# Kernel optimization log

Measured on AMD Instinct MI355X. Metric: run time of the kernel, lower is better.

Reference implementation:

```python
import jax, jax.numpy as jnp
import numpy as np
from jax import lax

D_MODEL = 1024
D_STATE = 128
D_CONV = 4
EXPAND = 2
N_HEADS = 32
CHUNK = 64
D_INNER = EXPAND * D_MODEL                 # 2048
CONV_DIM = D_INNER + 2 * D_STATE           # 2304
D_IN_PROJ = 2 * D_INNER + 2 * D_STATE + N_HEADS  # 4384
HEAD_DIM = D_INNER // N_HEADS              # 64
EPS = 1e-5


def setup_inputs() -> dict:
    key = jax.random.key(0)
    ks = jax.random.split(key, 10)
    u = jax.random.normal(ks[0], (4, 4096, D_MODEL), dtype=jnp.float32)
    in_proj_w = jax.random.normal(ks[1], (D_IN_PROJ, D_MODEL), dtype=jnp.float32) * 0.02
    conv_w = jax.random.normal(ks[2], (CONV_DIM, 1, D_CONV), dtype=jnp.float32) * 0.3
    conv_b = jnp.zeros((CONV_DIM,), dtype=jnp.float32)
    dt_bias = jax.random.uniform(ks[3], (N_HEADS,), minval=-0.5, maxval=0.5, dtype=jnp.float32)
    A_log = jax.random.uniform(ks[4], (N_HEADS,), minval=-0.1, maxval=-0.01, dtype=jnp.float32)
    D = jax.random.uniform(ks[5], (N_HEADS,), minval=0.9, maxval=1.1, dtype=jnp.float32)
    norm_w = jnp.ones((D_INNER,), dtype=jnp.float32)
    out_proj_w = jax.random.normal(ks[6], (D_MODEL, D_INNER), dtype=jnp.float32) * 0.02
    return {"u": u, "in_proj_w": in_proj_w, "conv_w": conv_w, "conv_b": conv_b,
            "dt_bias": dt_bias, "A_log": A_log, "D": D, "norm_w": norm_w,
            "out_proj_w": out_proj_w}


def segsum(x):
    """Stable segment sum. x: (..., T) -> (..., T, T); exp of it is 1-semiseparable."""
    T = x.shape[-1]
    xe = jnp.broadcast_to(x[..., :, None], x.shape + (T,))  # '... d -> ... d e'
    mask_strict = jnp.tril(jnp.ones((T, T), dtype=bool), k=-1)
    xe = jnp.where(mask_strict, xe, 0.0)
    seg = jnp.cumsum(xe, axis=-2)
    mask_incl = jnp.tril(jnp.ones((T, T), dtype=bool), k=0)
    return jnp.where(mask_incl, seg, -jnp.inf)


def ssd(x, A, B, C):
    """x:(b,L,h,p)  A:(b,L,h)  B,C:(b,L,h,n). L multiple of CHUNK."""
    b, Lp, h, p = x.shape
    n = B.shape[-1]
    c = Lp // CHUNK
    x = x.reshape(b, c, CHUNK, h, p)
    A = A.reshape(b, c, CHUNK, h).transpose(0, 3, 1, 2)       # (b,h,c,l)
    B = B.reshape(b, c, CHUNK, h, n)
    C = C.reshape(b, c, CHUNK, h, n)
    A_cumsum = jnp.cumsum(A, axis=-1)                          # (b,h,c,l)
    L = jnp.exp(segsum(A))                                     # (b,h,c,l,l)
    # intra-chunk (diagonal blocks)
    Y_diag = jnp.einsum('bclhn,bcshn,bhcls,bcshp->bclhp', C, B, L, x)
    # chunk-final states
    decay_states = jnp.exp(A_cumsum[:, :, :, -1:] - A_cumsum)  # (b,h,c,l)
    states = jnp.einsum('bclhn,bhcl,bclhp->bchpn', B, decay_states, x)
    init = jnp.zeros_like(states[:, :1])
    states = jnp.concatenate([init, states], axis=1)           # (b,c+1,h,p,n)
    decay_chunk = jnp.exp(segsum(jnp.pad(A_cumsum[:, :, :, -1], ((0, 0), (0, 0), (1, 0)))))
    new_states = jnp.einsum('bhzc,bchpn->bzhpn', decay_chunk, states)
    states, final_state = new_states[:, :-1], new_states[:, -1]
    # inter-chunk (off-diagonal) contribution
    state_decay_out = jnp.exp(A_cumsum)
    Y_off = jnp.einsum('bclhn,bchpn,bhcl->bclhp', C, states, state_decay_out)
    Y = (Y_diag + Y_off).reshape(b, Lp, h, p)
    return Y, final_state


def _forward(u, in_proj_w, conv_w, conv_b, dt_bias, A_log, D, norm_w, out_proj_w):
    b, seq_len, _ = u.shape
    pad = CHUNK - seq_len % CHUNK  # note: full extra chunk when seq_len % CHUNK == 0 (faithful)
    u = jnp.pad(u, ((0, 0), (0, pad), (0, 0)))
    Lp = u.shape[1]
    A = -jnp.exp(A_log)                                        # (h,)
    zxbcdt = jnp.einsum('bld,ed->ble', u, in_proj_w)           # (b,Lp,D_IN_PROJ)
    z = zxbcdt[..., :D_INNER]
    xBC = zxbcdt[..., D_INNER:D_INNER + CONV_DIM]
    dt = zxbcdt[..., -N_HEADS:]
    # causal depthwise conv1d + silu
    xc = xBC.transpose(0, 2, 1)                                # (b,conv_dim,Lp)
    xc = lax.conv_general_dilated(xc, conv_w, window_strides=(1,),
                                  padding=[(D_CONV - 1, 0)],
                                  feature_group_count=CONV_DIM,
                                  dimension_numbers=('NCH', 'OIH', 'NCH'))
    xBC = jax.nn.silu((xc + conv_b[None, :, None]).transpose(0, 2, 1))
    x = xBC[..., :D_INNER].reshape(b, Lp, N_HEADS, HEAD_DIM)
    Bm = xBC[..., D_INNER:D_INNER + D_STATE]
    Cm = xBC[..., D_INNER + D_STATE:]
    Bm = jnp.broadcast_to(Bm[:, :, None, :], (b, Lp, N_HEADS, D_STATE))
    Cm = jnp.broadcast_to(Cm[:, :, None, :], (b, Lp, N_HEADS, D_STATE))
    dt = jax.nn.softplus(dt + dt_bias)                         # (b,Lp,h)
    y, _ = ssd(x * dt[..., None], A * dt, Bm, Cm)
    y = y + x * D[None, None, :, None]
    y = y.reshape(b, Lp, D_INNER)
    # gated RMSNorm
    t = y * jax.nn.silu(z)
    t = t * jax.lax.rsqrt(jnp.mean(t * t, axis=-1, keepdims=True) + EPS) * norm_w
    out = jnp.einsum('bld,ed->ble', t, out_proj_w)
    return out[:, :seq_len]


def reference(u, in_proj_w, conv_w, conv_b, dt_bias, A_log, D, norm_w, out_proj_w):
    return _forward(u, in_proj_w, conv_w, conv_b, dt_bias, A_log, D, norm_w, out_proj_w)
```

## Files before the change

kernel.cpp:

```cpp
#include <hip/hip_runtime.h>
#include <hip/hip_bf16.h>
#include <math.h>


#define BL    16384
#define NCONV 2304
#define LDXP  2336

typedef __hip_bfloat16 bf16;
typedef __attribute__((ext_vector_type(8))) short bf16x8_i;
typedef __attribute__((ext_vector_type(4))) float f32x4;

union BF8 { uint4 u; bf16 h[8]; };
union BF2 { uint u; bf16 h[2]; };

__device__ __forceinline__ void gload_lds16(const void* g, void* l) {
  __builtin_amdgcn_global_load_lds(
      (__attribute__((address_space(1))) void*)(uintptr_t)g,
      (__attribute__((address_space(3))) void*)(uint32_t)(uintptr_t)l,
      16, 0, 0);
}

template<typename TC, bool CLAMPB>
__global__ __launch_bounds__(256) void gemm_bt_mfma(
    const bf16* __restrict__ A, int lda,
    const bf16* __restrict__ B, int ldb,
    TC* __restrict__ C, int ldc, int N, int K)
{
  __shared__ __align__(16) bf16 As2[2][128 * 64];
  __shared__ __align__(16) bf16 Bs2[2][128 * 64];
  const int tid  = threadIdx.x;
  const int lane = tid & 63;
  const int wid  = tid >> 6;

  const int gx  = gridDim.x;
  const int nwg = gx * gridDim.y;
  const int q   = nwg >> 3;
  int id = blockIdx.y * gx + blockIdx.x;
  id = (id & 7) * q + (id >> 3);
  const int bm = (id / gx) * 128;
  const int bn = (id % gx) * 128;

  const int wr = (wid >> 1) * 64;
  const int wc = (wid & 1) * 64;

  f32x4 acc[4][4] = {};

  int aoff[4][2], boff[4][2];
  #pragma unroll
  for (int i = 0; i < 4; ++i) {
    const int ar = wr + i * 16 + (lane & 15);
    const int br = wc + i * 16 + (lane & 15);
    const int asw = ((ar >> 1) & 7) << 3;
    const int bsw = ((br >> 1) & 7) << 3;
    #pragma unroll
    for (int ks = 0; ks < 2; ++ks) {
      const int c0 = ks * 32 + (lane >> 4) * 8;
      aoff[i][ks] = ar * 64 + (c0 ^ asw);
      boff[i][ks] = br * 64 + (c0 ^ bsw);
    }
  }

  const int srow = tid >> 3;
  const int sj   = tid & 7;
  const bf16* pA[4];
  const bf16* pB[4];
  #pragma unroll
  for (int i = 0; i < 4; ++i) {
    const int r  = i * 32 + srow;
    const int js = sj ^ ((r >> 1) & 7);
    int brow = bn + r;
    if (CLAMPB) brow = min(brow, N - 1);
    pA[i] = A + (size_t)(bm + r) * lda + js * 8;
    pB[i] = B + (size_t)brow * ldb + js * 8;
  }

  const int NT = K >> 6;
  #pragma unroll
  for (int i = 0; i < 4; ++i) {
    gload_lds16(pA[i], &As2[0][0] + i * 2048 + wid * 512);
    gload_lds16(pB[i], &Bs2[0][0] + i * 2048 + wid * 512);
    pA[i] += 64; pB[i] += 64;
  }

  for (int t = 0; t < NT; ++t) {
    const int cur = t & 1;
    if (t + 1 < NT) {
      bf16* dA = &As2[cur ^ 1][0];
      bf16* dB = &Bs2[cur ^ 1][0];
      #pragma unroll
      for (int i = 0; i < 4; ++i) {
        gload_lds16(pA[i], dA + i * 2048 + wid * 512);
        gload_lds16(pB[i], dB + i * 2048 + wid * 512);
        pA[i] += 64; pB[i] += 64;
      }
      asm volatile("s_waitcnt vmcnt(8)" ::: "memory");
    } else {
      asm volatile("s_waitcnt vmcnt(0)" ::: "memory");
    }
    __builtin_amdgcn_sched_barrier(0);
    __builtin_amdgcn_s_barrier();
    const bf16* Ab = &As2[cur][0];
    const bf16* Bb = &Bs2[cur][0];
    __builtin_amdgcn_s_setprio(1);
    #pragma unroll
    for (int ks = 0; ks < 2; ++ks) {
      bf16x8_i af[4], bfr[4];
      #pragma unroll
      for (int i = 0; i < 4; ++i) {
        af[i]  = *(const bf16x8_i*)(Ab + aoff[i][ks]);
        bfr[i] = *(const bf16x8_i*)(Bb + boff[i][ks]);
      }
      #pragma unroll
      for (int i = 0; i < 4; ++i)
        #pragma unroll
        for (int j = 0; j < 4; ++j)
          acc[i][j] = __builtin_amdgcn_mfma_f32_16x16x32_bf16(
              af[i], bfr[j], acc[i][j], 0, 0, 0);
    }
    __builtin_amdgcn_s_setprio(0);
    __builtin_amdgcn_s_barrier();
  }

  const int cr = (lane >> 4) * 4;
  const int cc = lane & 15;
  #pragma unroll
  for (int i = 0; i < 4; ++i) {
    #pragma unroll
    for (int j = 0; j < 4; ++j) {
      const int n = bn + wc + j * 16 + cc;
      if (n < N) {
        #pragma unroll
        for (int r = 0; r < 4; ++r) {
          const int m = bm + wr + i * 16 + cr + r;
          if constexpr (sizeof(TC) == 2)
            ((bf16*)C)[(size_t)m * ldc + n] = __float2bfloat16(acc[i][j][r]);
          else
            ((float*)C)[(size_t)m * ldc + n] = acc[i][j][r];
        }
      }
    }
  }
}

__global__ __launch_bounds__(256) void cvt_f32_bf16(
    const float* __restrict__ in, bf16* __restrict__ out)
{
  const size_t i = (size_t)(blockIdx.x * 256 + threadIdx.x) * 8;
  float4 a = *(const float4*)(in + i);
  float4 b = *(const float4*)(in + i + 4);
  BF8 o;
  o.h[0] = __float2bfloat16(a.x); o.h[1] = __float2bfloat16(a.y);
  o.h[2] = __float2bfloat16(a.z); o.h[3] = __float2bfloat16(a.w);
  o.h[4] = __float2bfloat16(b.x); o.h[5] = __float2bfloat16(b.y);
  o.h[6] = __float2bfloat16(b.z); o.h[7] = __float2bfloat16(b.w);
  *(uint4*)(out + i) = o.u;
}

__global__ __launch_bounds__(256) void dtsp_atot_kernel(
    const bf16* __restrict__ xpre, const float* __restrict__ dt_bias,
    const float* __restrict__ A_log,
    float* __restrict__ dtT, float* __restrict__ Atot)
{
  const int c = blockIdx.x, b = blockIdx.y;
  const int tid = threadIdx.x;
  const int h = tid & 31, lg = tid >> 5;
  __shared__ float red[8][33];
  float s = 0.f, vals[8];
  const bf16* src = xpre + ((size_t)b * 4096 + c * 64 + lg * 8) * LDXP + 2304 + h;
  const float bias = dt_bias[h];
  #pragma unroll
  for (int k = 0; k < 8; ++k) {
    float v = __bfloat162float(src[(size_t)k * LDXP]) + bias;
    v = fmaxf(v, 0.f) + log1pf(expf(-fabsf(v)));
    vals[k] = v; s += v;
  }
  float* dp = dtT + ((size_t)(b * 32 + h)) * 4096 + c * 64 + lg * 8;
  #pragma unroll
  for (int k = 0; k < 8; ++k) dp[k] = vals[k];
  red[lg][h] = s;
  __syncthreads();
  if (tid < 32) {
    float t = 0.f;
    #pragma unroll
    for (int g = 0; g < 8; ++g) t += red[g][tid];
    Atot[((size_t)b * 64 + c) * 32 + tid] = -expf(A_log[tid]) * t;
  }
}

__global__ __launch_bounds__(256) void conv_silu_kernel(
    const bf16* __restrict__ xpre,
    const float* __restrict__ conv_w,
    const float* __restrict__ conv_b,
    bf16* __restrict__ xBC)
{
  const int ch = blockIdx.x * 256 + threadIdx.x;
  const int t0 = blockIdx.y * 8;
  const int bb = blockIdx.z;
  const float w0 = conv_w[ch*4+0], w1 = conv_w[ch*4+1];
  const float w2 = conv_w[ch*4+2], w3 = conv_w[ch*4+3];
  const float bias = conv_b[ch];
  const size_t rb = (size_t)bb * 4096;
  const bf16* src = xpre + ch;
  float v0 = (t0 >= 3) ? __bfloat162float(src[(rb + t0 - 3) * LDXP]) : 0.f;
  float v1 = (t0 >= 2) ? __bfloat162float(src[(rb + t0 - 2) * LDXP]) : 0.f;
  float v2 = (t0 >= 1) ? __bfloat162float(src[(rb + t0 - 1) * LDXP]) : 0.f;
  for (int t = t0; t < t0 + 8; ++t) {
    float v3 = __bfloat162float(src[(rb + t) * LDXP]);
    float o = bias + w0*v0 + w1*v1 + w2*v2 + w3*v3;
    o = o / (1.f + expf(-o));
    xBC[(rb + t) * NCONV + ch] = __float2bfloat16(o);
    v0 = v1; v1 = v2; v2 = v3;
  }
}

__device__ __forceinline__ int swz8(int row) { return ((row >> 3) & 7) << 3; }

__global__ __launch_bounds__(256) void s0_scores(
    const bf16* __restrict__ xBC, float* __restrict__ sc_raw)
{
  const int c = blockIdx.x, b = blockIdx.y;
  const int tid = threadIdx.x, lane = tid & 63, wid = tid >> 6;
  __shared__ bf16 Bc[64 * 136];
  __shared__ bf16 Cc[64 * 136];
  const size_t r0 = (size_t)b * 4096 + (size_t)c * 64;
  #pragma unroll
  for (int k = 0; k < 4; ++k) {
    int id = tid + k * 256, l = id >> 4, n0 = (id & 15) * 8;
    *(uint4*)(Bc + l * 136 + n0) =
        *(const uint4*)(xBC + (r0 + l) * NCONV + 2048 + n0);
    *(uint4*)(Cc + l * 136 + n0) =
        *(const uint4*)(xBC + (r0 + l) * NCONV + 2176 + n0);
  }
  __syncthreads();
  const int wr  = (wid & 1) * 32;
  const int wcs = (wid >> 1) * 32;
  f32x4 as[2][2] = {};
  #pragma unroll
  for (int ks = 0; ks < 4; ++ks) {
    const int k0 = ks * 32 + (lane >> 4) * 8;
    bf16x8_i af[2], bfr[2];
    #pragma unroll
    for (int i = 0; i < 2; ++i)
      af[i] = *(const bf16x8_i*)(Cc + (wr + i * 16 + (lane & 15)) * 136 + k0);
    #pragma unroll
    for (int j = 0; j < 2; ++j)
      bfr[j] = *(const bf16x8_i*)(Bc + (wcs + j * 16 + (lane & 15)) * 136 + k0);
    #pragma unroll
    for (int i = 0; i < 2; ++i)
      #pragma unroll
      for (int j = 0; j < 2; ++j)
        as[i][j] = __builtin_amdgcn_mfma_f32_16x16x32_bf16(
            af[i], bfr[j], as[i][j], 0, 0, 0);
  }
  float* dst = sc_raw + ((size_t)(b * 64 + c)) * 4096;
  const int cr = (lane >> 4) * 4, cc = lane & 15;
  #pragma unroll
  for (int i = 0; i < 2; ++i)
    #pragma unroll
    for (int r = 0; r < 4; ++r) {
      const int l = wr + i * 16 + cr + r;
      #pragma unroll
      for (int j = 0; j < 2; ++j)
        dst[l * 64 + wcs + j * 16 + cc] = as[i][j][r];
    }
}

__global__ __launch_bounds__(256) void s1_localstate(
    const bf16* __restrict__ xBC, const float* __restrict__ dtT,
    const float* __restrict__ A_log, bf16* __restrict__ states, int b)
{
  const int hh = blockIdx.x, c = blockIdx.y;
  const int tid = threadIdx.x, lane = tid & 63, wid = tid >> 6;
  __shared__ bf16 BT[128 * 72];
  __shared__ bf16 xwT[64 * 72];
  __shared__ bf16 Sout[64 * 136];
  const size_t r0 = (size_t)b * 4096 + (size_t)c * 64;

  BF8 regB[4], regx[2];
  #pragma unroll
  for (int k = 0; k < 4; ++k) {
    int id = tid + k * 256, l = id >> 4, n0 = (id & 15) * 8;
    regB[k].u = *(const uint4*)(xBC + (r0 + l) * NCONV + 2048 + n0);
  }
  #pragma unroll
  for (int k = 0; k < 2; ++k) {
    int id = tid + k * 256, l = id >> 3, p0 = (id & 7) * 8;
    regx[k].u = *(const uint4*)(xBC + (r0 + l) * NCONV + hh * 64 + p0);
  }

  float d = dtT[((size_t)(b * 32 + hh)) * 4096 + c * 64 + lane];
  float Ah = -expf(A_log[hh]);
  float v = Ah * d;
  #pragma unroll
  for (int off = 1; off < 64; off <<= 1) {
    float up = __shfl_up(v, off, 64);
    if (lane >= off) v += up;
  }
  const float At = __shfl(v, 63, 64);
  const float w = d * __expf(At - v);

  #pragma unroll
  for (int k = 0; k < 4; ++k) {
    int id = tid + k * 256, l = id >> 4, n0 = (id & 15) * 8;
    #pragma unroll
    for (int j = 0; j < 8; ++j) {
      int n = n0 + j;
      BT[n * 72 + (l ^ swz8(n))] = regB[k].h[j];
    }
  }
  #pragma unroll
  for (int k = 0; k < 2; ++k) {
    int id = tid + k * 256, l = id >> 3, p0 = (id & 7) * 8;
    float wv = __shfl(w, l, 64);
    #pragma unroll
    for (int j = 0; j < 8; ++j) {
      int p = p0 + j;
      xwT[p * 72 + (l ^ swz8(p))] =
          __float2bfloat16(__bfloat162float(regx[k].h[j]) * wv);
    }
  }
  __syncthreads();

  const int wr = (wid & 1) * 32;
  const int wc = (wid >> 1) * 64;
  f32x4 acc[2][4] = {};
  #pragma unroll
  for (int ks = 0; ks < 2; ++ks) {
    const int k0 = ks * 32 + (lane >> 4) * 8;
    bf16x8_i a[2], bb[4];
    #pragma unroll
    for (int i = 0; i < 2; ++i) {
      int p = wr + i * 16 + (lane & 15);
      a[i] = *(const bf16x8_i*)(xwT + p * 72 + (k0 ^ swz8(p)));
    }
    #pragma unroll
    for (int j = 0; j < 4; ++j) {
      int n = wc + j * 16 + (lane & 15);
      bb[j] = *(const bf16x8_i*)(BT + n * 72 + (k0 ^ swz8(n)));
    }
    #pragma unroll
    for (int i = 0; i < 2; ++i)
      #pragma unroll
      for (int j = 0; j < 4; ++j)
        acc[i][j] = __builtin_amdgcn_mfma_f32_16x16x32_bf16(
            a[i], bb[j], acc[i][j], 0, 0, 0);
  }

  const int cr = (lane >> 4) * 4, cn = lane & 15;
  #pragma unroll
  for (int i = 0; i < 2; ++i)
    #pragma unroll
    for (int j = 0; j < 4; ++j)
      #pragma unroll
      for (int r = 0; r < 4; ++r)
        Sout[(wr + i * 16 + cr + r) * 136 + (wc + j * 16 + cn)] =
            __float2bfloat16(acc[i][j][r]);
  __syncthreads();
  bf16* sb = states + ((size_t)c * 32 + hh) * 8192;
  #pragma unroll
  for (int k = 0; k < 4; ++k) {
    int id = tid + k * 256, p = id >> 4, n0 = (id & 15) * 8;
    *(uint4*)(sb + p * 128 + n0) = *(const uint4*)(Sout + p * 136 + n0);
  }
}

__global__ __launch_bounds__(256) void s2_scan(
    bf16* __restrict__ states, const float* __restrict__ Atot, int b)
{
  const int h  = blockIdx.x >> 4;
  const int p  = ((blockIdx.x & 15) << 2) | (threadIdx.x >> 6);
  const int n0 = (threadIdx.x & 63) * 2;
  __shared__ float ec[64];
  if (threadIdx.x < 64)
    ec[threadIdx.x] = expf(Atot[((size_t)b * 64 + threadIdx.x) * 32 + h]);
  __syncthreads();
  bf16* ptr = states + ((size_t)h * 64 + p) * 128 + n0;
  const size_t cs = (size_t)32 * 8192;
  float ca = 0.f, cb = 0.f;
  BF2 g0, g1, g2, g3, q0, q1, q2, q3;
  g0.u = *(const uint*)(ptr + 0 * cs);
  g1.u = *(const uint*)(ptr + 1 * cs);
  g2.u = *(const uint*)(ptr + 2 * cs);
  g3.u = *(const uint*)(ptr + 3 * cs);
  for (int g = 0; g < 16; ++g) {
    const int c0 = g * 4;
    if (g < 15) {
      q0.u = *(const uint*)(ptr + (c0 + 4) * cs);
      q1.u = *(const uint*)(ptr + (c0 + 5) * cs);
      q2.u = *(const uint*)(ptr + (c0 + 6) * cs);
      q3.u = *(const uint*)(ptr + (c0 + 7) * cs);
    }
    BF2 o0, o1, o2, o3;
    const float e0 = ec[c0], e1 = ec[c0+1], e2 = ec[c0+2], e3 = ec[c0+3];
    o0.h[0] = __float2bfloat16(ca); o0.h[1] = __float2bfloat16(cb);
    ca = fmaf(e0, ca, __bfloat162float(g0.h[0]));
    cb = fmaf(e0, cb, __bfloat162float(g0.h[1]));
    o1.h[0] = __float2bfloat16(ca); o1.h[1] = __float2bfloat16(cb);
    ca = fmaf(e1, ca, __bfloat162float(g1.h[0]));
    cb = fmaf(e1, cb, __bfloat162float(g1.h[1]));
    o2.h[0] = __float2bfloat16(ca); o2.h[1] = __float2bfloat16(cb);
    ca = fmaf(e2, ca, __bfloat162float(g2.h[0]));
    cb = fmaf(e2, cb, __bfloat162float(g2.h[1]));
    o3.h[0] = __float2bfloat16(ca); o3.h[1] = __float2bfloat16(cb);
    ca = fmaf(e3, ca, __bfloat162float(g3.h[0]));
    cb = fmaf(e3, cb, __bfloat162float(g3.h[1]));
    *(uint*)(ptr + (c0 + 0) * cs) = o0.u;
    *(uint*)(ptr + (c0 + 1) * cs) = o1.u;
    *(uint*)(ptr + (c0 + 2) * cs) = o2.u;
    *(uint*)(ptr + (c0 + 3) * cs) = o3.u;
    g0 = q0; g1 = q1; g2 = q2; g3 = q3;
  }
}

__global__ __launch_bounds__(256) void s3_output(
    const bf16* __restrict__ xBC, const float* __restrict__ dtT,
    const float* __restrict__ A_log, const float* __restrict__ Dp,
    const bf16* __restrict__ states, const float* __restrict__ sc_raw,
    bf16* __restrict__ Y, int b)
{
  const int hh = blockIdx.x, c = blockIdx.y;
  const int tid = threadIdx.x, lane = tid & 63, wid = tid >> 6;
  __shared__ bf16 Cc[64 * 136];
  __shared__ bf16 Yb[64 * 136];
  __shared__ bf16 Sin[64 * 136];
  __shared__ bf16 xT[64 * 72];
  __shared__ bf16 scb[64 * 72];
  __shared__ float Ac[64], dts[64];
  const size_t r0 = (size_t)b * 4096 + (size_t)c * 64;

  if (tid < 64) {
    float d = dtT[((size_t)(b * 32 + hh)) * 4096 + c * 64 + tid];
    float Ah = -expf(A_log[hh]);
    float v = Ah * d;
    #pragma unroll
    for (int off = 1; off < 64; off <<= 1) {
      float up = __shfl_up(v, off, 64);
      if (tid >= off) v += up;
    }
    Ac[tid] = v; dts[tid] = d;
  }

  #pragma unroll
  for (int k = 0; k < 4; ++k) {
    int id = tid + k * 256, l = id >> 4, n0 = (id & 15) * 8;
    *(uint4*)(Cc + l * 136 + n0) =
        *(const uint4*)(xBC + (r0 + l) * NCONV + 2176 + n0);
  }
  const bf16* sb = states + ((size_t)c * 32 + hh) * 8192;
  #pragma unroll
  for (int k = 0; k < 4; ++k) {
    int id = tid + k * 256, p = id >> 4, n0 = (id & 15) * 8;
    *(uint4*)(Sin + p * 136 + n0) = *(const uint4*)(sb + p * 128 + n0);
  }
  #pragma unroll
  for (int k = 0; k < 2; ++k) {
    int id = tid + k * 256, l = id >> 3, p0 = (id & 7) * 8;
    BF8 v; v.u = *(const uint4*)(xBC + (r0 + l) * NCONV + hh * 64 + p0);
    #pragma unroll
    for (int j = 0; j < 8; ++j) {
      int p = p0 + j;
      xT[p * 72 + (l ^ swz8(p))] = v.h[j];
    }
  }
  __syncthreads();

  const int wr  = (wid & 1) * 32;
  const int wcs = (wid >> 1) * 32;
  bf16x8_i afrag[2][4];
  #pragma unroll
  for (int ks = 0; ks < 4; ++ks) {
    const int k0 = ks * 32 + (lane >> 4) * 8;
    #pragma unroll
    for (int i = 0; i < 2; ++i)
      afrag[i][ks] =
          *(const bf16x8_i*)(Cc + (wr + i * 16 + (lane & 15)) * 136 + k0);
  }
  {
    const float* scr = sc_raw + ((size_t)(b * 64 + c)) * 4096;
    #pragma unroll
    for (int k = 0; k < 4; ++k) {
      int idx = tid + k * 256;
      int l = idx >> 4, s0 = (idx & 15) * 4;
      float4 v = *(const float4*)(scr + l * 64 + s0);
      const float acl = Ac[l];
      float vv[4] = {v.x, v.y, v.z, v.w};
      #pragma unroll
      for (int j = 0; j < 4; ++j) {
        int s = s0 + j;
        float val = (s <= l) ? vv[j] * __expf(acl - Ac[s]) * dts[s] : 0.f;
        scb[l * 72 + s] = __float2bfloat16(val);
      }
    }
  }
  __syncthreads();

  f32x4 ay[2][2] = {};
  #pragma unroll
  for (int ks = 0; ks < 4; ++ks) {
    const int k0 = ks * 32 + (lane >> 4) * 8;
    #pragma unroll
    for (int j = 0; j < 2; ++j) {
      bf16x8_i bfr =
          *(const bf16x8_i*)(Sin + (wcs + j * 16 + (lane & 15)) * 136 + k0);
      #pragma unroll
      for (int i = 0; i < 2; ++i)
        ay[i][j] = __builtin_amdgcn_mfma_f32_16x16x32_bf16(
            afrag[i][ks], bfr, ay[i][j], 0, 0, 0);
    }
  }
  const int cr = (lane >> 4) * 4, cc = lane & 15;
  #pragma unroll
  for (int i = 0; i < 2; ++i)
    #pragma unroll
    for (int r = 0; r < 4; ++r) {
      const float dk = __expf(Ac[wr + i * 16 + cr + r]);
      #pragma unroll
      for (int j = 0; j < 2; ++j) ay[i][j][r] *= dk;
    }
  #pragma unroll
  for (int ks = 0; ks < 2; ++ks) {
    const int k0 = ks * 32 + (lane >> 4) * 8;
    bf16x8_i a2[2], b2[2];
    #pragma unroll
    for (int i = 0; i < 2; ++i)
      a2[i] = *(const bf16x8_i*)(scb + (wr + i * 16 + (lane & 15)) * 72 + k0);
    #pragma unroll
    for (int j = 0; j < 2; ++j) {
      int p = wcs + j * 16 + (lane & 15);
      b2[j] = *(const bf16x8_i*)(xT + p * 72 + (k0 ^ swz8(p)));
    }
    #pragma unroll
    for (int i = 0; i < 2; ++i)
      #pragma unroll
      for (int j = 0; j < 2; ++j)
        ay[i][j] = __builtin_amdgcn_mfma_f32_16x16x32_bf16(
            a2[i], b2[j], ay[i][j], 0, 0, 0);
  }
  const float Dh = Dp[hh];
  #pragma unroll
  for (int i = 0; i < 2; ++i)
    #pragma unroll
    for (int r = 0; r < 4; ++r) {
      const int l = wr + i * 16 + cr + r;
      #pragma unroll
      for (int j = 0; j < 2; ++j) {
        const int p = wcs + j * 16 + cc;
        float xv = __bfloat162float(xT[p * 72 + (l ^ swz8(p))]);
        Yb[l * 136 + p] = __float2bfloat16(ay[i][j][r] + Dh * xv);
      }
    }
  __syncthreads();
  #pragma unroll
  for (int k = 0; k < 2; ++k) {
    int id = tid + k * 256, l = id >> 3, p0 = (id & 7) * 8;
    *(uint4*)(Y + (r0 + l) * 2048 + hh * 64 + p0) =
        *(const uint4*)(Yb + l * 136 + p0);
  }
}

__global__ __launch_bounds__(256) void gate_rmsnorm_kernel(
    bf16* __restrict__ y, const bf16* __restrict__ z,
    const float* __restrict__ norm_w)
{
  const size_t row = blockIdx.x;
  const int tid = threadIdx.x;
  __shared__ float red[4];
  const bf16* zr = z + row * 2048;
  bf16* yr = y + row * 2048;
  BF8 zv, yv;
  zv.u = *(const uint4*)(zr + tid * 8);
  yv.u = *(const uint4*)(yr + tid * 8);
  float t[8];
  float local = 0.f;
  #pragma unroll
  for (int j = 0; j < 8; ++j) {
    float zz = __bfloat162float(zv.h[j]);
    float yy = __bfloat162float(yv.h[j]);
    float tv = yy * (zz / (1.f + expf(-zz)));
    t[j] = tv;
    local += tv * tv;
  }
  #pragma unroll
  for (int off = 32; off; off >>= 1) local += __shfl_down(local, off, 64);
  if ((tid & 63) == 0) red[tid >> 6] = local;
  __syncthreads();
  const float total = red[0] + red[1] + red[2] + red[3];
  const float scale = rsqrtf(total * (1.f / 2048.f) + 1e-5f);
  BF8 o;
  #pragma unroll
  for (int j = 0; j < 8; ++j)
    o.h[j] = __float2bfloat16(t[j] * scale * norm_w[tid * 8 + j]);
  *(uint4*)(yr + tid * 8) = o.u;
}

extern "C" void kernel_launch(void* const* d_in, const int* in_sizes, int n_in,
                              void* d_out, int out_size, void* d_ws, size_t ws_size,
                              hipStream_t stream) {
  (void)in_sizes; (void)n_in; (void)out_size; (void)ws_size;
  const float* u          = (const float*)d_in[0];
  const float* in_proj_w  = (const float*)d_in[1];
  const float* conv_w     = (const float*)d_in[2];
  const float* conv_b     = (const float*)d_in[3];
  const float* dt_bias    = (const float*)d_in[4];
  const float* A_log      = (const float*)d_in[5];
  const float* Dp         = (const float*)d_in[6];
  const float* norm_w     = (const float*)d_in[7];
  const float* out_proj_w = (const float*)d_in[8];
  float* out = (float*)d_out;

  char* ws = (char*)d_ws;
  bf16*  u_bf   = (bf16*)ws;
  bf16*  xpre   = (bf16*)(ws + 33554432);
  bf16*  xBCc   = (bf16*)(ws + 110100480);
  float* dtT    = (float*)(ws + 185597952);
  bf16*  W_xpre = (bf16*)(ws + 187695104);
  bf16*  W_z    = (bf16*)(ws + 192479232);
  bf16*  w_out  = (bf16*)(ws + 196673536);
  float* Atot   = (float*)(ws + 200867840);
  bf16*  states = (bf16*)(ws + 200900608);
  bf16*  ybuf   = xpre;
  bf16*  zbuf   = xBCc;
  float* sc_raw = (float*)(ws + 100663296);

  cvt_f32_bf16<<<dim3(8192), 256, 0, stream>>>(u, u_bf);
  cvt_f32_bf16<<<dim3(1168), 256, 0, stream>>>(in_proj_w + (size_t)2048*1024,
                                               W_xpre);
  cvt_f32_bf16<<<dim3(1024), 256, 0, stream>>>(in_proj_w, W_z);
  cvt_f32_bf16<<<dim3(1024), 256, 0, stream>>>(out_proj_w, w_out);
  gemm_bt_mfma<bf16, true><<<dim3(19, 128), 256, 0, stream>>>(
      u_bf, 1024, W_xpre, 1024, xpre, LDXP, 2336, 1024);
  dtsp_atot_kernel<<<dim3(64, 4), 256, 0, stream>>>(xpre, dt_bias, A_log,
                                                    dtT, Atot);
  conv_silu_kernel<<<dim3(9, 512, 4), 256, 0, stream>>>(xpre, conv_w, conv_b,
                                                        xBCc);
  s0_scores<<<dim3(64, 4), 256, 0, stream>>>(xBCc, sc_raw);
  for (int b = 0; b < 4; ++b) {
    s1_localstate<<<dim3(32, 64), 256, 0, stream>>>(xBCc, dtT, A_log,
                                                    states, b);
    s2_scan<<<dim3(512), 256, 0, stream>>>(states, Atot, b);
    s3_output<<<dim3(32, 64), 256, 0, stream>>>(xBCc, dtT, A_log, Dp,
                                                states, sc_raw, ybuf, b);
  }
  gemm_bt_mfma<bf16, false><<<dim3(16, 128), 256, 0, stream>>>(
      u_bf, 1024, W_z, 1024, zbuf, 2048, 2048, 1024);
  gate_rmsnorm_kernel<<<dim3(BL), 256, 0, stream>>>(ybuf, zbuf, norm_w);
  gemm_bt_mfma<float, false><<<dim3(8, 128), 256, 0, stream>>>(
      ybuf, 2048, w_out, 2048, out, 1024, 1024, 2048);
}
```

Before: 521.7 us.

## Replace 128x128 GEMM with 256x256-tile 8-wave kernel and split-K-half pipelining

```diff
diff --git a/kernel.cpp b/kernel.cpp
--- a/kernel.cpp
+++ b/kernel.cpp
@@ -22,125 +22,177 @@
 }
 
 template<typename TC, bool CLAMPB>
-__global__ __launch_bounds__(256) void gemm_bt_mfma(
+__global__ __launch_bounds__(512) void gemm_bt_256(
     const bf16* __restrict__ A, int lda,
     const bf16* __restrict__ B, int ldb,
     TC* __restrict__ C, int ldc, int N, int K)
 {
-  __shared__ __align__(16) bf16 As2[2][128 * 64];
-  __shared__ __align__(16) bf16 Bs2[2][128 * 64];
+  __shared__ __align__(16) bf16 L[2][4][8192];
   const int tid  = threadIdx.x;
   const int lane = tid & 63;
   const int wid  = tid >> 6;
+  const int wm   = wid >> 2;
+  const int wn   = wid & 3;
 
   const int gx  = gridDim.x;
   const int nwg = gx * gridDim.y;
   const int q   = nwg >> 3;
   int id = blockIdx.y * gx + blockIdx.x;
   id = (id & 7) * q + (id >> 3);
-  const int bm = (id / gx) * 128;
-  const int bn = (id % gx) * 128;
-
-  const int wr = (wid >> 1) * 64;
-  const int wc = (wid & 1) * 64;
-
-  f32x4 acc[4][4] = {};
-
-  int aoff[4][2], boff[4][2];
-  #pragma unroll
-  for (int i = 0; i < 4; ++i) {
-    const int ar = wr + i * 16 + (lane & 15);
-    const int br = wc + i * 16 + (lane & 15);
-    const int asw = ((ar >> 1) & 7) << 3;
-    const int bsw = ((br >> 1) & 7) << 3;
-    #pragma unroll
-    for (int ks = 0; ks < 2; ++ks) {
-      const int c0 = ks * 32 + (lane >> 4) * 8;
-      aoff[i][ks] = ar * 64 + (c0 ^ asw);
-      boff[i][ks] = br * 64 + (c0 ^ bsw);
-    }
-  }
-
-  const int srow = tid >> 3;
-  const int sj   = tid & 7;
-  const bf16* pA[4];
-  const bf16* pB[4];
-  #pragma unroll
-  for (int i = 0; i < 4; ++i) {
-    const int r  = i * 32 + srow;
-    const int js = sj ^ ((r >> 1) & 7);
-    int brow = bn + r;
-    if (CLAMPB) brow = min(brow, N - 1);
-    pA[i] = A + (size_t)(bm + r) * lda + js * 8;
-    pB[i] = B + (size_t)brow * ldb + js * 8;
+  const int bm = (id / gx) * 256;
+  const int bn = (id % gx) * 256;
+
+  f32x4 acc[8][4] = {};
+
+  int aofs[2][4], bofs[4];
+  #pragma unroll
+  for (int fh = 0; fh < 2; ++fh)
+    #pragma unroll
+    for (int mf = 0; mf < 4; ++mf) {
+      const int ar = wm * 128 + fh * 64 + mf * 16 + (lane & 15);
+      aofs[fh][mf] = ar * 32 + (((lane >> 4) ^ ((ar >> 1) & 3)) << 3);
+    }
+  #pragma unroll
+  for (int nf = 0; nf < 4; ++nf) {
+    const int br = wn * 64 + nf * 16 + (lane & 15);
+    bofs[nf] = br * 32 + (((lane >> 4) ^ ((br >> 1) & 3)) << 3);
   }
 
   const int NT = K >> 6;
-  #pragma unroll
-  for (int i = 0; i < 4; ++i) {
-    gload_lds16(pA[i], &As2[0][0] + i * 2048 + wid * 512);
-    gload_lds16(pB[i], &Bs2[0][0] + i * 2048 + wid * 512);
-    pA[i] += 64; pB[i] += 64;
-  }
-
-  for (int t = 0; t < NT; ++t) {
-    const int cur = t & 1;
-    if (t + 1 < NT) {
-      bf16* dA = &As2[cur ^ 1][0];
-      bf16* dB = &Bs2[cur ^ 1][0];
-      #pragma unroll
-      for (int i = 0; i < 4; ++i) {
-        gload_lds16(pA[i], dA + i * 2048 + wid * 512);
-        gload_lds16(pB[i], dB + i * 2048 + wid * 512);
-        pA[i] += 64; pB[i] += 64;
-      }
-      asm volatile("s_waitcnt vmcnt(8)" ::: "memory");
-    } else {
-      asm volatile("s_waitcnt vmcnt(0)" ::: "memory");
-    }
+  const int srow = tid >> 2;
+  const int sblk = tid & 3;
+
+  auto stageA = [&](int tile, int kh) {
+    const int kt = min(tile, NT - 1);
+    const int k0 = kt * 64 + kh * 32;
+    bf16* dst = &L[tile & 1][kh][0];
+    #pragma unroll
+    for (int i = 0; i < 2; ++i) {
+      const int r = i * 128 + srow;
+      const int blk = sblk ^ ((r >> 1) & 3);
+      gload_lds16(A + (size_t)(bm + r) * lda + k0 + blk * 8,
+                  dst + i * 4096 + wid * 512);
+    }
+  };
+  auto stageB = [&](int tile, int kh) {
+    const int kt = min(tile, NT - 1);
+    const int k0 = kt * 64 + kh * 32;
+    bf16* dst = &L[tile & 1][2 + kh][0];
+    #pragma unroll
+    for (int i = 0; i < 2; ++i) {
+      const int r = i * 128 + srow;
+      const int blk = sblk ^ ((r >> 1) & 3);
+      int grow = bn + r;
+      if (CLAMPB) grow = min(grow, N - 1);
+      gload_lds16(B + (size_t)grow * ldb + k0 + blk * 8,
+                  dst + i * 4096 + wid * 512);
+    }
+  };
+
+  stageA(0, 0); stageB(0, 0); stageA(0, 1); stageB(0, 1);
+  stageA(1, 0); stageB(1, 0);
+
+  for (int T = 0; T < NT; ++T) {
+    const int buf = T & 1;
+    const bf16* A0r = &L[buf][0][0];
+    const bf16* A1r = &L[buf][1][0];
+    const bf16* B0r = &L[buf][2][0];
+    const bf16* B1r = &L[buf][3][0];
+    bf16x8_i bfr[4], af[4];
+
+    stageA(T + 1, 1);
+    asm volatile("s_waitcnt vmcnt(10)" ::: "memory");
     __builtin_amdgcn_sched_barrier(0);
     __builtin_amdgcn_s_barrier();
-    const bf16* Ab = &As2[cur][0];
-    const bf16* Bb = &Bs2[cur][0];
+    #pragma unroll
+    for (int mf = 0; mf < 4; ++mf) af[mf] = *(const bf16x8_i*)(A0r + aofs[0][mf]);
+    #pragma unroll
+    for (int nf = 0; nf < 4; ++nf) bfr[nf] = *(const bf16x8_i*)(B0r + bofs[nf]);
+    asm volatile("s_waitcnt lgkmcnt(0)" ::: "memory");
+    __builtin_amdgcn_sched_barrier(0);
     __builtin_amdgcn_s_setprio(1);
     #pragma unroll
-    for (int ks = 0; ks < 2; ++ks) {
-      bf16x8_i af[4], bfr[4];
-      #pragma unroll
-      for (int i = 0; i < 4; ++i) {
-        af[i]  = *(const bf16x8_i*)(Ab + aoff[i][ks]);
-        bfr[i] = *(const bf16x8_i*)(Bb + boff[i][ks]);
-      }
-      #pragma unroll
-      for (int i = 0; i < 4; ++i)
-        #pragma unroll
-        for (int j = 0; j < 4; ++j)
-          acc[i][j] = __builtin_amdgcn_mfma_f32_16x16x32_bf16(
-              af[i], bfr[j], acc[i][j], 0, 0, 0);
-    }
+    for (int mf = 0; mf < 4; ++mf)
+      #pragma unroll
+      for (int nf = 0; nf < 4; ++nf)
+        acc[mf][nf] = __builtin_amdgcn_mfma_f32_16x16x32_bf16(
+            af[mf], bfr[nf], acc[mf][nf], 0, 0, 0);
     __builtin_amdgcn_s_setprio(0);
     __builtin_amdgcn_s_barrier();
+
+    stageB(T + 1, 1);
+    #pragma unroll
+    for (int mf = 0; mf < 4; ++mf) af[mf] = *(const bf16x8_i*)(A0r + aofs[1][mf]);
+    asm volatile("s_waitcnt lgkmcnt(0)" ::: "memory");
+    __builtin_amdgcn_sched_barrier(0);
+    __builtin_amdgcn_s_setprio(1);
+    #pragma unroll
+    for (int mf = 0; mf < 4; ++mf)
+      #pragma unroll
+      for (int nf = 0; nf < 4; ++nf)
+        acc[4 + mf][nf] = __builtin_amdgcn_mfma_f32_16x16x32_bf16(
+            af[mf], bfr[nf], acc[4 + mf][nf], 0, 0, 0);
+    __builtin_amdgcn_s_setprio(0);
+    __builtin_amdgcn_s_barrier();
+
+    stageA(T + 2, 0);
+    asm volatile("s_waitcnt vmcnt(10)" ::: "memory");
+    __builtin_amdgcn_sched_barrier(0);
+    __builtin_amdgcn_s_barrier();
+    #pragma unroll
+    for (int mf = 0; mf < 4; ++mf) af[mf] = *(const bf16x8_i*)(A1r + aofs[0][mf]);
+    #pragma unroll
+    for (int nf = 0; nf < 4; ++nf) bfr[nf] = *(const bf16x8_i*)(B1r + bofs[nf]);
+    asm volatile("s_waitcnt lgkmcnt(0)" ::: "memory");
+    __builtin_amdgcn_sched_barrier(0);
+    __builtin_amdgcn_s_setprio(1);
+    #pragma unroll
+    for (int mf = 0; mf < 4; ++mf)
+      #pragma unroll
+      for (int nf = 0; nf < 4; ++nf)
+        acc[mf][nf] = __builtin_amdgcn_mfma_f32_16x16x32_bf16(
+            af[mf], bfr[nf], acc[mf][nf], 0, 0, 0);
+    __builtin_amdgcn_s_setprio(0);
+    __builtin_amdgcn_s_barrier();
+
+    stageB(T + 2, 0);
+    #pragma unroll
+    for (int mf = 0; mf < 4; ++mf) af[mf] = *(const bf16x8_i*)(A1r + aofs[1][mf]);
+    asm volatile("s_waitcnt lgkmcnt(0)" ::: "memory");
+    __builtin_amdgcn_sched_barrier(0);
+    __builtin_amdgcn_s_setprio(1);
+    #pragma unroll
+    for (int mf = 0; mf < 4; ++mf)
+      #pragma unroll
+      for (int nf = 0; nf < 4; ++nf)
+        acc[4 + mf][nf] = __builtin_amdgcn_mfma_f32_16x16x32_bf16(
+            af[mf], bfr[nf], acc[4 + mf][nf], 0, 0, 0);
+    __builtin_amdgcn_s_setprio(0);
+    __builtin_amdgcn_s_barrier();
   }
 
   const int cr = (lane >> 4) * 4;
   const int cc = lane & 15;
   #pragma unroll
-  for (int i = 0; i < 4; ++i) {
-    #pragma unroll
-    for (int j = 0; j < 4; ++j) {
-      const int n = bn + wc + j * 16 + cc;
-      if (n < N) {
-        #pragma unroll
-        for (int r = 0; r < 4; ++r) {
-          const int m = bm + wr + i * 16 + cr + r;
-          if constexpr (sizeof(TC) == 2)
-            ((bf16*)C)[(size_t)m * ldc + n] = __float2bfloat16(acc[i][j][r]);
-          else
-            ((float*)C)[(size_t)m * ldc + n] = acc[i][j][r];
+  for (int fh = 0; fh < 2; ++fh)
+    #pragma unroll
+    for (int mf = 0; mf < 4; ++mf) {
+      #pragma unroll
+      for (int nf = 0; nf < 4; ++nf) {
+        const int n = bn + wn * 64 + nf * 16 + cc;
+        if (n < N) {
+          #pragma unroll
+          for (int r = 0; r < 4; ++r) {
+            const int m = bm + wm * 128 + fh * 64 + mf * 16 + cr + r;
+            if constexpr (sizeof(TC) == 2)
+              ((bf16*)C)[(size_t)m * ldc + n] =
+                  __float2bfloat16(acc[fh * 4 + mf][nf][r]);
+            else
+              ((float*)C)[(size_t)m * ldc + n] = acc[fh * 4 + mf][nf][r];
+          }
         }
       }
     }
-  }
 }
 
 __global__ __launch_bounds__(256) void cvt_f32_bf16(
@@ -628,7 +680,7 @@
                                                W_xpre);
   cvt_f32_bf16<<<dim3(1024), 256, 0, stream>>>(in_proj_w, W_z);
   cvt_f32_bf16<<<dim3(1024), 256, 0, stream>>>(out_proj_w, w_out);
-  gemm_bt_mfma<bf16, true><<<dim3(19, 128), 256, 0, stream>>>(
+  gemm_bt_256<bf16, true><<<dim3(10, 64), 512, 0, stream>>>(
       u_bf, 1024, W_xpre, 1024, xpre, LDXP, 2336, 1024);
   dtsp_atot_kernel<<<dim3(64, 4), 256, 0, stream>>>(xpre, dt_bias, A_log,
                                                     dtT, Atot);
@@ -642,9 +694,9 @@
     s3_output<<<dim3(32, 64), 256, 0, stream>>>(xBCc, dtT, A_log, Dp,
                                                 states, sc_raw, ybuf, b);
   }
-  gemm_bt_mfma<bf16, false><<<dim3(16, 128), 256, 0, stream>>>(
+  gemm_bt_256<bf16, false><<<dim3(8, 64), 512, 0, stream>>>(
       u_bf, 1024, W_z, 1024, zbuf, 2048, 2048, 1024);
   gate_rmsnorm_kernel<<<dim3(BL), 256, 0, stream>>>(ybuf, zbuf, norm_w);
-  gemm_bt_mfma<float, false><<<dim3(8, 128), 256, 0, stream>>>(
+  gemm_bt_256<float, false><<<dim3(4, 64), 512, 0, stream>>>(
       ybuf, 2048, w_out, 2048, out, 1024, 1024, 2048);
 }
```

Measured after the change: 525.3 us. Within noise of the previous version (+0.7%).

## Batch SSD chunk-state kernels over two batches per launch and deepen scan prefetch

Applied to the files above, without the earlier changes.

```diff
diff --git a/kernel.cpp b/kernel.cpp
--- a/kernel.cpp
+++ b/kernel.cpp
@@ -6,6 +6,7 @@
 #define BL    16384
 #define NCONV 2304
 #define LDXP  2336
+#define STATE_ELEMS 16777216ull
 
 typedef __hip_bfloat16 bf16;
 typedef __attribute__((ext_vector_type(8))) short bf16x8_i;
@@ -268,9 +269,10 @@
 
 __global__ __launch_bounds__(256) void s1_localstate(
     const bf16* __restrict__ xBC, const float* __restrict__ dtT,
-    const float* __restrict__ A_log, bf16* __restrict__ states, int b)
+    const float* __restrict__ A_log, bf16* __restrict__ states, int bbase)
 {
   const int hh = blockIdx.x, c = blockIdx.y;
+  const int b  = bbase + blockIdx.z;
   const int tid = threadIdx.x, lane = tid & 63, wid = tid >> 6;
   __shared__ bf16 BT[128 * 72];
   __shared__ bf16 xwT[64 * 72];
@@ -357,7 +359,8 @@
         Sout[(wr + i * 16 + cr + r) * 136 + (wc + j * 16 + cn)] =
             __float2bfloat16(acc[i][j][r]);
   __syncthreads();
-  bf16* sb = states + ((size_t)c * 32 + hh) * 8192;
+  bf16* sb = states + (size_t)blockIdx.z * STATE_ELEMS
+                    + ((size_t)c * 32 + hh) * 8192;
   #pragma unroll
   for (int k = 0; k < 4; ++k) {
     int id = tid + k * 256, p = id >> 4, n0 = (id & 15) * 8;
@@ -365,51 +368,47 @@
   }
 }
 
+#define S2STEP(R, CI)                                                     \
+  {                                                                       \
+    BF2 o;                                                                \
+    o.h[0] = __float2bfloat16(ca); o.h[1] = __float2bfloat16(cb);         \
+    const float e = ec[CI];                                               \
+    ca = fmaf(e, ca, __bfloat162float(R.h[0]));                           \
+    cb = fmaf(e, cb, __bfloat162float(R.h[1]));                           \
+    *(uint*)(ptr + (size_t)(CI) * cs) = o.u;                              \
+    if ((CI) + 8 < 64) R.u = *(const uint*)(ptr + (size_t)((CI) + 8) * cs); \
+  }
+
 __global__ __launch_bounds__(256) void s2_scan(
-    bf16* __restrict__ states, const float* __restrict__ Atot, int b)
+    bf16* __restrict__ states, const float* __restrict__ Atot, int bbase)
 {
   const int h  = blockIdx.x >> 4;
   const int p  = ((blockIdx.x & 15) << 2) | (threadIdx.x >> 6);
   const int n0 = (threadIdx.x & 63) * 2;
+  const int b  = bbase + blockIdx.y;
   __shared__ float ec[64];
   if (threadIdx.x < 64)
     ec[threadIdx.x] = expf(Atot[((size_t)b * 64 + threadIdx.x) * 32 + h]);
   __syncthreads();
-  bf16* ptr = states + ((size_t)h * 64 + p) * 128 + n0;
+  bf16* ptr = states + (size_t)blockIdx.y * STATE_ELEMS
+                     + ((size_t)h * 64 + p) * 128 + n0;
   const size_t cs = (size_t)32 * 8192;
   float ca = 0.f, cb = 0.f;
-  BF2 g0, g1, g2, g3, q0, q1, q2, q3;
-  g0.u = *(const uint*)(ptr + 0 * cs);
-  g1.u = *(const uint*)(ptr + 1 * cs);
-  g2.u = *(const uint*)(ptr + 2 * cs);
-  g3.u = *(const uint*)(ptr + 3 * cs);
-  for (int g = 0; g < 16; ++g) {
-    const int c0 = g * 4;
-    if (g < 15) {
-      q0.u = *(const uint*)(ptr + (c0 + 4) * cs);
-      q1.u = *(const uint*)(ptr + (c0 + 5) * cs);
-      q2.u = *(const uint*)(ptr + (c0 + 6) * cs);
-      q3.u = *(const uint*)(ptr + (c0 + 7) * cs);
-    }
-    BF2 o0, o1, o2, o3;
-    const float e0 = ec[c0], e1 = ec[c0+1], e2 = ec[c0+2], e3 = ec[c0+3];
-    o0.h[0] = __float2bfloat16(ca); o0.h[1] = __float2bfloat16(cb);
-    ca = fmaf(e0, ca, __bfloat162float(g0.h[0]));
-    cb = fmaf(e0, cb, __bfloat162float(g0.h[1]));
-    o1.h[0] = __float2bfloat16(ca); o1.h[1] = __float2bfloat16(cb);
-    ca = fmaf(e1, ca, __bfloat162float(g1.h[0]));
-    cb = fmaf(e1, cb, __bfloat162float(g1.h[1]));
-    o2.h[0] = __float2bfloat16(ca); o2.h[1] = __float2bfloat16(cb);
-    ca = fmaf(e2, ca, __bfloat162float(g2.h[0]));
-    cb = fmaf(e2, cb, __bfloat162float(g2.h[1]));
-    o3.h[0] = __float2bfloat16(ca); o3.h[1] = __float2bfloat16(cb);
-    ca = fmaf(e3, ca, __bfloat162float(g3.h[0]));
-    cb = fmaf(e3, cb, __bfloat162float(g3.h[1]));
-    *(uint*)(ptr + (c0 + 0) * cs) = o0.u;
-    *(uint*)(ptr + (c0 + 1) * cs) = o1.u;
-    *(uint*)(ptr + (c0 + 2) * cs) = o2.u;
-    *(uint*)(ptr + (c0 + 3) * cs) = o3.u;
-    g0 = q0; g1 = q1; g2 = q2; g3 = q3;
+  BF2 r0, r1, r2, r3, r4, r5, r6, r7;
+  r0.u = *(const uint*)(ptr + 0 * cs);
+  r1.u = *(const uint*)(ptr + 1 * cs);
+  r2.u = *(const uint*)(ptr + 2 * cs);
+  r3.u = *(const uint*)(ptr + 3 * cs);
+  r4.u = *(const uint*)(ptr + 4 * cs);
+  r5.u = *(const uint*)(ptr + 5 * cs);
+  r6.u = *(const uint*)(ptr + 6 * cs);
+  r7.u = *(const uint*)(ptr + 7 * cs);
+  for (int g = 0; g < 8; ++g) {
+    const int c0 = g * 8;
+    S2STEP(r0, c0 + 0); S2STEP(r1, c0 + 1);
+    S2STEP(r2, c0 + 2); S2STEP(r3, c0 + 3);
+    S2STEP(r4, c0 + 4); S2STEP(r5, c0 + 5);
+    S2STEP(r6, c0 + 6); S2STEP(r7, c0 + 7);
   }
 }
 
@@ -417,9 +416,10 @@
     const bf16* __restrict__ xBC, const float* __restrict__ dtT,
     const float* __restrict__ A_log, const float* __restrict__ Dp,
     const bf16* __restrict__ states, const float* __restrict__ sc_raw,
-    bf16* __restrict__ Y, int b)
+    bf16* __restrict__ Y, int bbase)
 {
   const int hh = blockIdx.x, c = blockIdx.y;
+  const int b  = bbase + blockIdx.z;
   const int tid = threadIdx.x, lane = tid & 63, wid = tid >> 6;
   __shared__ bf16 Cc[64 * 136];
   __shared__ bf16 Yb[64 * 136];
@@ -447,7 +447,8 @@
     *(uint4*)(Cc + l * 136 + n0) =
         *(const uint4*)(xBC + (r0 + l) * NCONV + 2176 + n0);
   }
-  const bf16* sb = states + ((size_t)c * 32 + hh) * 8192;
+  const bf16* sb = states + (size_t)blockIdx.z * STATE_ELEMS
+                          + ((size_t)c * 32 + hh) * 8192;
   #pragma unroll
   for (int k = 0; k < 4; ++k) {
     int id = tid + k * 256, p = id >> 4, n0 = (id & 15) * 8;
@@ -597,7 +598,7 @@
 extern "C" void kernel_launch(void* const* d_in, const int* in_sizes, int n_in,
                               void* d_out, int out_size, void* d_ws, size_t ws_size,
                               hipStream_t stream) {
-  (void)in_sizes; (void)n_in; (void)out_size; (void)ws_size;
+  (void)in_sizes; (void)n_in; (void)out_size;
   const float* u          = (const float*)d_in[0];
   const float* in_proj_w  = (const float*)d_in[1];
   const float* conv_w     = (const float*)d_in[2];
@@ -614,20 +615,21 @@
   bf16*  xpre   = (bf16*)(ws + 33554432);
   bf16*  xBCc   = (bf16*)(ws + 110100480);
   float* dtT    = (float*)(ws + 185597952);
-  bf16*  W_xpre = (bf16*)(ws + 187695104);
-  bf16*  W_z    = (bf16*)(ws + 192479232);
-  bf16*  w_out  = (bf16*)(ws + 196673536);
+  bf16*  W_all  = (bf16*)(ws + 187695104);
+  bf16*  W_z    = W_all;
+  bf16*  W_xpre = W_all + (size_t)2048 * 1024;
+  bf16*  out_w  = (bf16*)(ws + 196673536);
   float* Atot   = (float*)(ws + 200867840);
   bf16*  states = (bf16*)(ws + 200900608);
   bf16*  ybuf   = xpre;
   bf16*  zbuf   = xBCc;
   float* sc_raw = (float*)(ws + 100663296);
 
+  const int NB = (ws_size >= 268009472ull) ? 2 : 1;
+
   cvt_f32_bf16<<<dim3(8192), 256, 0, stream>>>(u, u_bf);
-  cvt_f32_bf16<<<dim3(1168), 256, 0, stream>>>(in_proj_w + (size_t)2048*1024,
-                                               W_xpre);
-  cvt_f32_bf16<<<dim3(1024), 256, 0, stream>>>(in_proj_w, W_z);
-  cvt_f32_bf16<<<dim3(1024), 256, 0, stream>>>(out_proj_w, w_out);
+  cvt_f32_bf16<<<dim3(2192), 256, 0, stream>>>(in_proj_w, W_all);
+  cvt_f32_bf16<<<dim3(1024), 256, 0, stream>>>(out_proj_w, out_w);
   gemm_bt_mfma<bf16, true><<<dim3(19, 128), 256, 0, stream>>>(
       u_bf, 1024, W_xpre, 1024, xpre, LDXP, 2336, 1024);
   dtsp_atot_kernel<<<dim3(64, 4), 256, 0, stream>>>(xpre, dt_bias, A_log,
@@ -635,16 +637,16 @@
   conv_silu_kernel<<<dim3(9, 512, 4), 256, 0, stream>>>(xpre, conv_w, conv_b,
                                                         xBCc);
   s0_scores<<<dim3(64, 4), 256, 0, stream>>>(xBCc, sc_raw);
-  for (int b = 0; b < 4; ++b) {
-    s1_localstate<<<dim3(32, 64), 256, 0, stream>>>(xBCc, dtT, A_log,
-                                                    states, b);
-    s2_scan<<<dim3(512), 256, 0, stream>>>(states, Atot, b);
-    s3_output<<<dim3(32, 64), 256, 0, stream>>>(xBCc, dtT, A_log, Dp,
-                                                states, sc_raw, ybuf, b);
+  for (int b0 = 0; b0 < 4; b0 += NB) {
+    s1_localstate<<<dim3(32, 64, NB), 256, 0, stream>>>(xBCc, dtT, A_log,
+                                                        states, b0);
+    s2_scan<<<dim3(512, NB), 256, 0, stream>>>(states, Atot, b0);
+    s3_output<<<dim3(32, 64, NB), 256, 0, stream>>>(xBCc, dtT, A_log, Dp,
+                                                    states, sc_raw, ybuf, b0);
   }
   gemm_bt_mfma<bf16, false><<<dim3(16, 128), 256, 0, stream>>>(
       u_bf, 1024, W_z, 1024, zbuf, 2048, 2048, 1024);
   gate_rmsnorm_kernel<<<dim3(BL), 256, 0, stream>>>(ybuf, zbuf, norm_w);
   gemm_bt_mfma<float, false><<<dim3(8, 128), 256, 0, stream>>>(
-      ybuf, 2048, w_out, 2048, out, 1024, 1024, 2048);
-}
+      ybuf, 2048, out_w, 2048, out, 1024, 1024, 2048);
+}
```

Measured after the change: 503.5 us, median of 2. -3.5%, faster.
